# Kernel tuning notes

Hardware: AMD Instinct MI355X
Metric: run time of the kernel (lower is better)

The kernel has to match this reference:

```python
import jax, jax.numpy as jnp
import numpy as np

E = 1024
H = 16
DH = E // H
EPS = 1e-09


def setup_inputs() -> dict:
    key = jax.random.key(0)
    ks = jax.random.split(key, 12)
    B, S = 2, 2048
    scale = 1.0 / np.sqrt(E)
    inp = {
        "query": jax.random.normal(ks[0], (B, S, E), dtype=jnp.float32),
        "key": jax.random.normal(ks[1], (B, S, E), dtype=jnp.float32),
        "value": jax.random.normal(ks[2], (B, S, E), dtype=jnp.float32),
        "mask": jax.random.randint(ks[3], (B, 1, S, S), 0, 2, dtype=jnp.int32),
        "Wq": jax.random.normal(ks[4], (E, E), dtype=jnp.float32) * scale,
        "bq": jnp.zeros((E,), dtype=jnp.float32),
        "Wk": jax.random.normal(ks[5], (E, E), dtype=jnp.float32) * scale,
        "bk": jnp.zeros((E,), dtype=jnp.float32),
        "Wv": jax.random.normal(ks[6], (E, E), dtype=jnp.float32) * scale,
        "bv": jnp.zeros((E,), dtype=jnp.float32),
        "Wo": jax.random.normal(ks[7], (E, E), dtype=jnp.float32) * scale,
        "bo": jnp.zeros((E,), dtype=jnp.float32),
    }
    return inp


def _split_heads(x):
    # [B,S,E] -> [B,H,S,DH]
    B, S, _ = x.shape
    return x.reshape(B, S, H, DH).transpose(0, 2, 1, 3)


def reference(query, key, value, mask, Wq, bq, Wk, bk, Wv, bv, Wo, bo):
    q = _split_heads(query @ Wq.T + bq)
    k = _split_heads(key @ Wk.T + bk)
    v = _split_heads(value @ Wv.T + bv)
    # scores: [B,H,Sq,Sk]; NOTE: original module applies NO softmax.
    scores = jnp.einsum("bhqd,bhkd->bhqk", q, k) / np.sqrt(DH)
    # masked_fill_(mask == 0, epsilon): replace masked positions with 1e-9
    scores = jnp.where(mask == 0, jnp.float32(EPS), scores)
    # dropout p=0.0 (eval) -> identity
    out = jnp.einsum("bhqk,bhkd->bhqd", scores, v)
    B, _, S, _ = out.shape
    out = out.transpose(0, 2, 1, 3).reshape(B, S, E)
    return out @ Wo.T + bo
```

## Files before the change

### kernel.cpp

```cpp
#include <hip/hip_runtime.h>
#include <hip/hip_bf16.h>
#include <stdint.h>
#include <stddef.h>

#define SB 2
#define SS 2048
#define SE 1024
#define SH 16
#define SD 64

typedef __attribute__((ext_vector_type(8))) short bf16x8;
typedef __attribute__((ext_vector_type(4))) float f32x4;

__device__ __forceinline__ short f2bf(float f) {
    union { float f; uint32_t u; } v; v.f = f;
    uint32_t u = v.u;
    uint32_t r = (u + 0x7fffu + ((u >> 16) & 1u)) >> 16;
    return (short)(uint16_t)r;
}

struct CvtArgs {
    const float* src[7];
    short* dst[7];
    int nblk[7];
};

__global__ __launch_bounds__(256) void cvt_bf16(CvtArgs a) {
    const int j = blockIdx.y;
    if (blockIdx.x >= a.nblk[j]) return;
    const size_t i = ((size_t)blockIdx.x * 256 + threadIdx.x) * 8;
    const float* s = a.src[j] + i;
    f32x4 f0 = *(const f32x4*)s;
    f32x4 f1 = *(const f32x4*)(s + 4);
    bf16x8 o;
    o[0] = f2bf(f0[0]); o[1] = f2bf(f0[1]); o[2] = f2bf(f0[2]); o[3] = f2bf(f0[3]);
    o[4] = f2bf(f1[0]); o[5] = f2bf(f1[1]); o[6] = f2bf(f1[2]); o[7] = f2bf(f1[3]);
    *(bf16x8*)(a.dst[j] + i) = o;
}

__global__ __launch_bounds__(256) void pack_mask(const int* __restrict__ m,
                                                 unsigned long long* __restrict__ mp) {
    const int lane = threadIdx.x & 63;
    int wv = (blockIdx.x * 256 + threadIdx.x) >> 6;
    const int NW = SB * SS * (SS / 64);
    const int stride = (gridDim.x * 256) >> 6;
    for (int wd = wv; wd < NW; wd += stride) {
        int v = m[(size_t)wd * 64 + lane];
        unsigned long long b = __ballot(v != 0);
        if (lane == 0) mp[wd] = b;
    }
}

struct GemmJob {
    const short* A; const short* W; const float* bias; void* C;
    int mode;
    float scale;
};

template <bool OUTF32>
__global__ __launch_bounds__(256, 4) void gemm_bf(GemmJob j0, GemmJob j1, GemmJob j2) {
    GemmJob j = (blockIdx.z == 0) ? j0 : (blockIdx.z == 1) ? j1 : j2;
    __shared__ __align__(16) short As[64][72];
    __shared__ __align__(16) short Bs[128][72];

    const int m0 = blockIdx.y * 64;
    const int n0 = blockIdx.x * 128;
    const int tid = threadIdx.x;
    const int lane = tid & 63;
    const int w = tid >> 6;
    const int wm = (w >> 1) * 32;
    const int wn = (w & 1) * 64;
    const int quad = lane >> 4;
    const int l16 = lane & 15;

    f32x4 acc[2][4] = {};
    bf16x8 pa[2], pw[4];

    auto prefetch = [&](int k0) {
#pragma unroll
        for (int r = 0; r < 2; ++r) {
            int c = tid + r * 256; int row = c >> 3; int col = (c & 7) * 8;
            pa[r] = *(const bf16x8*)(j.A + (size_t)(m0 + row) * 1024 + k0 + col);
        }
#pragma unroll
        for (int r = 0; r < 4; ++r) {
            int c = tid + r * 256; int row = c >> 3; int col = (c & 7) * 8;
            pw[r] = *(const bf16x8*)(j.W + (size_t)(n0 + row) * 1024 + k0 + col);
        }
    };

    prefetch(0);
    for (int k0 = 0; k0 < 1024; k0 += 64) {
#pragma unroll
        for (int r = 0; r < 2; ++r) {
            int c = tid + r * 256; int row = c >> 3; int col = (c & 7) * 8;
            *(bf16x8*)&As[row][col] = pa[r];
        }
#pragma unroll
        for (int r = 0; r < 4; ++r) {
            int c = tid + r * 256; int row = c >> 3; int col = (c & 7) * 8;
            *(bf16x8*)&Bs[row][col] = pw[r];
        }
        __syncthreads();
        if (k0 + 64 < 1024) prefetch(k0 + 64);
#pragma unroll
        for (int ks = 0; ks < 2; ++ks) {
            bf16x8 af[2], bfr[4];
#pragma unroll
            for (int mi = 0; mi < 2; ++mi)
                af[mi] = *(const bf16x8*)&As[wm + mi * 16 + l16][ks * 32 + quad * 8];
#pragma unroll
            for (int ni = 0; ni < 4; ++ni)
                bfr[ni] = *(const bf16x8*)&Bs[wn + ni * 16 + l16][ks * 32 + quad * 8];
#pragma unroll
            for (int mi = 0; mi < 2; ++mi)
#pragma unroll
                for (int ni = 0; ni < 4; ++ni)
                    acc[mi][ni] = __builtin_amdgcn_mfma_f32_16x16x32_bf16(
                        af[mi], bfr[ni], acc[mi][ni], 0, 0, 0);
        }
        __syncthreads();
    }

#pragma unroll
    for (int mi = 0; mi < 2; ++mi) {
#pragma unroll
        for (int ni = 0; ni < 4; ++ni) {
            int n = n0 + wn + ni * 16 + l16;
            float bv = j.bias[n];
#pragma unroll
            for (int r = 0; r < 4; ++r) {
                int m = m0 + wm + mi * 16 + quad * 4 + r;
                float v = (acc[mi][ni][r] + bv) * j.scale;
                if (OUTF32) {
                    ((float*)j.C)[(size_t)m * 1024 + n] = v;
                } else {
                    short o = f2bf(v);
                    short* C = (short*)j.C;
                    if (j.mode == 0) {
                        C[(size_t)m * 1024 + n] = o;
                    } else {
                        int b = m >> 11, s = m & 2047;
                        int hh = n >> 6, d = n & 63;
                        if (j.mode == 1)
                            C[(((size_t)(b * SH + hh) * SS) + s) * SD + d] = o;
                        else
                            C[(((size_t)(b * SH + hh) * SD) + d) * SS + s] = o;
                    }
                }
            }
        }
    }
}

__global__ __launch_bounds__(256, 2) void attn_nosoftmax(
    const short* __restrict__ Q,
    const short* __restrict__ Kk,
    const short* __restrict__ Vt,
    const unsigned long long* __restrict__ Mp,
    short* __restrict__ O) {
    __shared__ __align__(16) short Ks[128][72];
    __shared__ __align__(16) short Ssm[128 * 136];

    const int bh = blockIdx.y;
    const int qt = blockIdx.x;
    const int b = bh >> 4;
    const int h = bh & 15;
    const int q0 = qt * 128;

    const short* qbase = Q + (size_t)bh * SS * SD;
    const short* kbase = Kk + (size_t)bh * SS * SD;
    const short* vbase = Vt + (size_t)bh * SD * SS;
    const unsigned long long* mbase = Mp + (size_t)b * SS * (SS / 64);

    const int tid = threadIdx.x;
    const int lane = tid & 63;
    const int w = tid >> 6;
    const int quad = lane >> 4;
    const int l16 = lane & 15;
    const int wm = (w >> 1) * 64;
    const int wn = (w & 1) * 64;

    bf16x8 qa[4][2];
#pragma unroll
    for (int mi = 0; mi < 4; ++mi)
#pragma unroll
        for (int ks = 0; ks < 2; ++ks)
            qa[mi][ks] = *(const bf16x8*)(qbase +
                (size_t)(q0 + wm + mi * 16 + l16) * SD + ks * 32 + quad * 8);

    f32x4 oacc[2][4] = {};
    const int pq = w * 32;

    bf16x8 kpf[4];
    auto kload = [&](int kk0) {
#pragma unroll
        for (int r = 0; r < 4; ++r) {
            int c = tid + r * 256; int row = c >> 3; int col = (c & 7) * 8;
            kpf[r] = *(const bf16x8*)(kbase + (size_t)(kk0 + row) * SD + col);
        }
    };
    auto kstore = [&]() {
#pragma unroll
        for (int r = 0; r < 4; ++r) {
            int c = tid + r * 256; int row = c >> 3; int col = (c & 7) * 8;
            *(bf16x8*)&Ks[row][col] = kpf[r];
        }
    };

    kload(0);
    kstore();
    __syncthreads();

    for (int k0 = 0; k0 < SS; k0 += 128) {
        int kpf0 = (k0 + 128 < SS) ? k0 + 128 : k0;
        kload(kpf0);

        f32x4 sacc[4][4] = {};
#pragma unroll
        for (int ks = 0; ks < 2; ++ks) {
            bf16x8 kb[4];
#pragma unroll
            for (int ni = 0; ni < 4; ++ni)
                kb[ni] = *(const bf16x8*)&Ks[wn + ni * 16 + l16][ks * 32 + quad * 8];
#pragma unroll
            for (int mi = 0; mi < 4; ++mi)
#pragma unroll
                for (int ni = 0; ni < 4; ++ni)
                    sacc[mi][ni] = __builtin_amdgcn_mfma_f32_16x16x32_bf16(
                        qa[mi][ks], kb[ni], sacc[mi][ni], 0, 0, 0);
        }

        const int mcol = ((k0 + wn) >> 6);
#pragma unroll
        for (int mi = 0; mi < 4; ++mi) {
            int qrow_l = wm + mi * 16 + quad * 4;
#pragma unroll
            for (int r = 0; r < 4; ++r) {
                unsigned long long mwd =
                    mbase[(size_t)(q0 + qrow_l + r) * (SS / 64) + mcol];
                unsigned long long sh = mwd >> l16;
                short* dst = &Ssm[(qrow_l + r) * 136 + wn + l16];
#pragma unroll
                for (int ni = 0; ni < 4; ++ni) {
                    uint32_t bit = (uint32_t)(sh >> (16 * ni)) & 1u;
                    float v = bit ? sacc[mi][ni][r] : 0.0f;
                    dst[ni * 16] = f2bf(v);
                }
            }
        }
        __syncthreads();

        kstore();

#pragma unroll
        for (int ks2 = 0; ks2 < 4; ++ks2) {
            bf16x8 sa[2], vb[4];
#pragma unroll
            for (int mi2 = 0; mi2 < 2; ++mi2)
                sa[mi2] = *(const bf16x8*)&Ssm[(pq + mi2 * 16 + l16) * 136 +
                                               ks2 * 32 + quad * 8];
#pragma unroll
            for (int ni = 0; ni < 4; ++ni)
                vb[ni] = *(const bf16x8*)(vbase + (size_t)(ni * 16 + l16) * SS +
                                          k0 + ks2 * 32 + quad * 8);
#pragma unroll
            for (int mi2 = 0; mi2 < 2; ++mi2)
#pragma unroll
                for (int ni = 0; ni < 4; ++ni)
                    oacc[mi2][ni] = __builtin_amdgcn_mfma_f32_16x16x32_bf16(
                        sa[mi2], vb[ni], oacc[mi2][ni], 0, 0, 0);
        }
        __syncthreads();
    }

#pragma unroll
    for (int mi2 = 0; mi2 < 2; ++mi2) {
#pragma unroll
        for (int ni = 0; ni < 4; ++ni) {
            int d = ni * 16 + l16;
#pragma unroll
            for (int r = 0; r < 4; ++r) {
                int qg = q0 + pq + mi2 * 16 + quad * 4 + r;
                O[((size_t)b * SS + qg) * SE + h * SD + d] =
                    f2bf(oacc[mi2][ni][r]);
            }
        }
    }
}

extern "C" void kernel_launch(void* const* d_in, const int* in_sizes, int n_in,
                              void* d_out, int out_size, void* d_ws,
                              size_t ws_size, hipStream_t stream) {
    const float* query = (const float*)d_in[0];
    const float* key   = (const float*)d_in[1];
    const float* value = (const float*)d_in[2];
    const int*   mask  = (const int*)d_in[3];
    float* out = (float*)d_out;

    const size_t NEL = (size_t)SB * SS * SE;
    unsigned long long* Mp = (unsigned long long*)d_out;
    short* mb   = (short*)d_in[3];
    short* qbf  = mb;
    short* kbf  = mb + NEL;
    short* vbf  = mb + 2 * NEL;
    short* Wqb  = mb + 3 * NEL;
    short* Wkb  = Wqb + SE * SE;
    short* Wvb  = Wkb + SE * SE;
    short* Wob  = Wvb + SE * SE;
    short* Qb   = (short*)d_in[0];
    short* Om   = (short*)d_in[0] + NEL;
    short* Kb   = (short*)d_in[1];
    short* Vtb  = (short*)d_in[2];

    dim3 tblk(256);

    pack_mask<<<dim3(1024), tblk, 0, stream>>>(mask, Mp);

    CvtArgs ca;
    ca.src[0] = query; ca.dst[0] = qbf; ca.nblk[0] = 2048;
    ca.src[1] = key;   ca.dst[1] = kbf; ca.nblk[1] = 2048;
    ca.src[2] = value; ca.dst[2] = vbf; ca.nblk[2] = 2048;
    ca.src[3] = (const float*)d_in[4];  ca.dst[3] = Wqb; ca.nblk[3] = 512;
    ca.src[4] = (const float*)d_in[6];  ca.dst[4] = Wkb; ca.nblk[4] = 512;
    ca.src[5] = (const float*)d_in[8];  ca.dst[5] = Wvb; ca.nblk[5] = 512;
    ca.src[6] = (const float*)d_in[10]; ca.dst[6] = Wob; ca.nblk[6] = 512;
    cvt_bf16<<<dim3(2048, 7), tblk, 0, stream>>>(ca);

    GemmJob jq{qbf, Wqb, (const float*)d_in[5], Qb,  1, 0.125f};
    GemmJob jv{vbf, Wvb, (const float*)d_in[9], Vtb, 2, 1.0f};
    GemmJob jk{kbf, Wkb, (const float*)d_in[7], Kb,  1, 1.0f};
    gemm_bf<false><<<dim3(8, 64, 3), tblk, 0, stream>>>(jq, jv, jk);

    attn_nosoftmax<<<dim3(SS / 128, SB * SH), tblk, 0, stream>>>(Qb, Kb, Vtb, Mp, Om);

    GemmJob jo{Om, Wob, (const float*)d_in[11], out, 0, 1.0f};
    gemm_bf<true><<<dim3(8, 64, 1), tblk, 0, stream>>>(jo, jo, jo);
}
```

Before: 325.0 us.

## Rewrite attention to register-resident scores and use direct-to-LDS GEMM loads

The attention kernel is restructured to 64-query tiles, one 16-row slab per wave. It computes S^T = K·Q^T so the masked scores can go straight from MFMA accumulators into the A operand of the PV MFMA, with no LDS round trip. K and V tiles are double-buffered in LDS, and the mask is packed transposed so each lane reads one contiguous 64-bit word. The projection GEMMs move to 128x128 tiles that load via global_load_lds. They drop the register prefetch and use an unpadded LDS layout, which risks bank conflicts and leaves load latency exposed between the two barriers.

Result: faster. 288.8 us (-11.1%).

```diff
diff --git a/kernel.cpp b/kernel.cpp
--- a/kernel.cpp
+++ b/kernel.cpp
@@ -17,6 +17,20 @@
     uint32_t u = v.u;
     uint32_t r = (u + 0x7fffu + ((u >> 16) & 1u)) >> 16;
     return (short)(uint16_t)r;
+}
+
+__device__ __forceinline__ uint32_t pkmask(float a, float b, uint32_t bits) {
+    union { float f; uint32_t u; } ua, ub;
+    ua.f = a; ub.f = b;
+    uint32_t ra = (bits & 1u) ? (ua.u + 0x7fffu + ((ua.u >> 16) & 1u)) : 0u;
+    uint32_t rb = (bits & 2u) ? (ub.u + 0x7fffu + ((ub.u >> 16) & 1u)) : 0u;
+    return (rb & 0xffff0000u) | (ra >> 16);
+}
+
+__device__ __forceinline__ void gld16(const short* g, short* l) {
+    __builtin_amdgcn_global_load_lds(
+        (const __attribute__((address_space(1))) unsigned int*)g,
+        (__attribute__((address_space(3))) unsigned int*)l, 16, 0, 0);
 }
 
 struct CvtArgs {
@@ -46,8 +60,13 @@
     const int stride = (gridDim.x * 256) >> 6;
     for (int wd = wv; wd < NW; wd += stride) {
         int v = m[(size_t)wd * 64 + lane];
-        unsigned long long b = __ballot(v != 0);
-        if (lane == 0) mp[wd] = b;
+        unsigned long long bb = __ballot(v != 0);
+        if (lane == 0) {
+            int b = wd >> 16;
+            int q = (wd >> 5) & 2047;
+            int kw = wd & 31;
+            mp[((size_t)b << 16) + kw * 2048 + q] = bb;
+        }
     }
 }
 
@@ -58,62 +77,44 @@
 };
 
 template <bool OUTF32>
-__global__ __launch_bounds__(256, 4) void gemm_bf(GemmJob j0, GemmJob j1, GemmJob j2) {
+__global__ __launch_bounds__(256, 3) void gemm128(GemmJob j0, GemmJob j1, GemmJob j2) {
     GemmJob j = (blockIdx.z == 0) ? j0 : (blockIdx.z == 1) ? j1 : j2;
-    __shared__ __align__(16) short As[64][72];
-    __shared__ __align__(16) short Bs[128][72];
-
-    const int m0 = blockIdx.y * 64;
+    __shared__ short As[128 * 64];
+    __shared__ short Bs[128 * 64];
+
+    const int m0 = blockIdx.y * 128;
     const int n0 = blockIdx.x * 128;
     const int tid = threadIdx.x;
     const int lane = tid & 63;
     const int w = tid >> 6;
-    const int wm = (w >> 1) * 32;
+    const int wm = (w >> 1) * 64;
     const int wn = (w & 1) * 64;
     const int quad = lane >> 4;
     const int l16 = lane & 15;
 
-    f32x4 acc[2][4] = {};
-    bf16x8 pa[2], pw[4];
-
-    auto prefetch = [&](int k0) {
-#pragma unroll
-        for (int r = 0; r < 2; ++r) {
-            int c = tid + r * 256; int row = c >> 3; int col = (c & 7) * 8;
-            pa[r] = *(const bf16x8*)(j.A + (size_t)(m0 + row) * 1024 + k0 + col);
-        }
-#pragma unroll
-        for (int r = 0; r < 4; ++r) {
-            int c = tid + r * 256; int row = c >> 3; int col = (c & 7) * 8;
-            pw[r] = *(const bf16x8*)(j.W + (size_t)(n0 + row) * 1024 + k0 + col);
-        }
-    };
-
-    prefetch(0);
+    f32x4 acc[4][4] = {};
+
     for (int k0 = 0; k0 < 1024; k0 += 64) {
 #pragma unroll
-        for (int r = 0; r < 2; ++r) {
-            int c = tid + r * 256; int row = c >> 3; int col = (c & 7) * 8;
-            *(bf16x8*)&As[row][col] = pa[r];
-        }
-#pragma unroll
-        for (int r = 0; r < 4; ++r) {
-            int c = tid + r * 256; int row = c >> 3; int col = (c & 7) * 8;
-            *(bf16x8*)&Bs[row][col] = pw[r];
+        for (int i = 0; i < 4; ++i) {
+            int ch = lane + 64 * (w * 4 + i);
+            int row = ch >> 3;
+            int col = (ch & 7) * 8;
+            gld16(j.A + (size_t)(m0 + row) * 1024 + k0 + col, &As[(w * 4 + i) * 512]);
+            gld16(j.W + (size_t)(n0 + row) * 1024 + k0 + col, &Bs[(w * 4 + i) * 512]);
         }
         __syncthreads();
-        if (k0 + 64 < 1024) prefetch(k0 + 64);
 #pragma unroll
         for (int ks = 0; ks < 2; ++ks) {
-            bf16x8 af[2], bfr[4];
-#pragma unroll
-            for (int mi = 0; mi < 2; ++mi)
-                af[mi] = *(const bf16x8*)&As[wm + mi * 16 + l16][ks * 32 + quad * 8];
+            bf16x8 af[4], bfr[4];
+#pragma unroll
+            for (int mi = 0; mi < 4; ++mi)
+                af[mi] = *(const bf16x8*)&As[(wm + mi * 16 + l16) * 64 + ks * 32 + quad * 8];
 #pragma unroll
             for (int ni = 0; ni < 4; ++ni)
-                bfr[ni] = *(const bf16x8*)&Bs[wn + ni * 16 + l16][ks * 32 + quad * 8];
-#pragma unroll
-            for (int mi = 0; mi < 2; ++mi)
+                bfr[ni] = *(const bf16x8*)&Bs[(wn + ni * 16 + l16) * 64 + ks * 32 + quad * 8];
+#pragma unroll
+            for (int mi = 0; mi < 4; ++mi)
 #pragma unroll
                 for (int ni = 0; ni < 4; ++ni)
                     acc[mi][ni] = __builtin_amdgcn_mfma_f32_16x16x32_bf16(
@@ -123,7 +124,7 @@
     }
 
 #pragma unroll
-    for (int mi = 0; mi < 2; ++mi) {
+    for (int mi = 0; mi < 4; ++mi) {
 #pragma unroll
         for (int ni = 0; ni < 4; ++ni) {
             int n = n0 + wn + ni * 16 + l16;
@@ -153,138 +154,116 @@
     }
 }
 
-__global__ __launch_bounds__(256, 2) void attn_nosoftmax(
+__global__ __launch_bounds__(256, 4) void attn2(
     const short* __restrict__ Q,
     const short* __restrict__ Kk,
     const short* __restrict__ Vt,
-    const unsigned long long* __restrict__ Mp,
+    const unsigned long long* __restrict__ MpT,
     short* __restrict__ O) {
-    __shared__ __align__(16) short Ks[128][72];
-    __shared__ __align__(16) short Ssm[128 * 136];
-
+    __shared__ __align__(16) short Ks[2][64 * 72];
+    __shared__ __align__(16) short Vs[2][64 * 72];
+
+    const int qt = blockIdx.x;
     const int bh = blockIdx.y;
-    const int qt = blockIdx.x;
     const int b = bh >> 4;
     const int h = bh & 15;
-    const int q0 = qt * 128;
+    const int q0 = qt * 64;
 
     const short* qbase = Q + (size_t)bh * SS * SD;
     const short* kbase = Kk + (size_t)bh * SS * SD;
     const short* vbase = Vt + (size_t)bh * SD * SS;
-    const unsigned long long* mbase = Mp + (size_t)b * SS * (SS / 64);
+    const unsigned long long* mTb = MpT + ((size_t)b << 16);
 
     const int tid = threadIdx.x;
     const int lane = tid & 63;
     const int w = tid >> 6;
     const int quad = lane >> 4;
     const int l16 = lane & 15;
-    const int wm = (w >> 1) * 64;
-    const int wn = (w & 1) * 64;
-
-    bf16x8 qa[4][2];
-#pragma unroll
-    for (int mi = 0; mi < 4; ++mi)
-#pragma unroll
-        for (int ks = 0; ks < 2; ++ks)
-            qa[mi][ks] = *(const bf16x8*)(qbase +
-                (size_t)(q0 + wm + mi * 16 + l16) * SD + ks * 32 + quad * 8);
-
-    f32x4 oacc[2][4] = {};
-    const int pq = w * 32;
-
-    bf16x8 kpf[4];
-    auto kload = [&](int kk0) {
+    const int qw = q0 + w * 16;
+
+    const bf16x8 qf0 = *(const bf16x8*)(qbase + (size_t)(qw + l16) * SD + quad * 8);
+    const bf16x8 qf1 = *(const bf16x8*)(qbase + (size_t)(qw + l16) * SD + 32 + quad * 8);
+
+    f32x4 oacc[4] = {};
+
+    bf16x8 kpf[2], vpf[2];
+    int prow[2], pcol[2];
+#pragma unroll
+    for (int r = 0; r < 2; ++r) {
+        int ch = tid + r * 256;
+        prow[r] = ch >> 3;
+        pcol[r] = (ch & 7) * 8;
+    }
+    auto loadKV = [&](int k0) {
+#pragma unroll
+        for (int r = 0; r < 2; ++r) {
+            kpf[r] = *(const bf16x8*)(kbase + (size_t)(k0 + prow[r]) * SD + pcol[r]);
+            vpf[r] = *(const bf16x8*)(vbase + (size_t)prow[r] * SS + k0 + pcol[r]);
+        }
+    };
+    auto storeKV = [&](int buf) {
+#pragma unroll
+        for (int r = 0; r < 2; ++r) {
+            *(bf16x8*)&Ks[buf][prow[r] * 72 + pcol[r]] = kpf[r];
+            *(bf16x8*)&Vs[buf][prow[r] * 72 + pcol[r]] = vpf[r];
+        }
+    };
+
+    loadKV(0);
+    int cur = 0;
+
+    for (int k0 = 0; k0 < SS; k0 += 64) {
+        storeKV(cur);
+        if (k0 + 64 < SS) loadKV(k0 + 64);
+        unsigned long long w64 = mTb[(k0 >> 6) * 2048 + qw + l16];
+        __syncthreads();
+
+        const short* KsB = &Ks[cur][0];
+        const short* VsB = &Vs[cur][0];
+#pragma unroll
+        for (int p = 0; p < 2; ++p) {
+            const int s0 = p * 2, s1 = p * 2 + 1;
+            bf16x8 a00 = *(const bf16x8*)&KsB[(s0 * 16 + l16) * 72 + quad * 8];
+            bf16x8 a01 = *(const bf16x8*)&KsB[(s0 * 16 + l16) * 72 + 32 + quad * 8];
+            bf16x8 a10 = *(const bf16x8*)&KsB[(s1 * 16 + l16) * 72 + quad * 8];
+            bf16x8 a11 = *(const bf16x8*)&KsB[(s1 * 16 + l16) * 72 + 32 + quad * 8];
+            f32x4 sA = {}, sB = {};
+            sA = __builtin_amdgcn_mfma_f32_16x16x32_bf16(a00, qf0, sA, 0, 0, 0);
+            sA = __builtin_amdgcn_mfma_f32_16x16x32_bf16(a01, qf1, sA, 0, 0, 0);
+            sB = __builtin_amdgcn_mfma_f32_16x16x32_bf16(a10, qf0, sB, 0, 0, 0);
+            sB = __builtin_amdgcn_mfma_f32_16x16x32_bf16(a11, qf1, sB, 0, 0, 0);
+
+            uint32_t sh0 = (uint32_t)(w64 >> (s0 * 16 + quad * 4));
+            uint32_t sh1 = (uint32_t)(w64 >> (s1 * 16 + quad * 4));
+            union { uint32_t d[4]; bf16x8 v; } scf;
+            scf.d[0] = pkmask(sA[0], sA[1], sh0);
+            scf.d[1] = pkmask(sA[2], sA[3], sh0 >> 2);
+            scf.d[2] = pkmask(sB[0], sB[1], sh1);
+            scf.d[3] = pkmask(sB[2], sB[3], sh1 >> 2);
+
+#pragma unroll
+            for (int di = 0; di < 4; ++di) {
+                union { uint32_t d[4]; bf16x8 v; } vb;
+                const uint32_t* vlo =
+                    (const uint32_t*)&VsB[(di * 16 + l16) * 72 + s0 * 16 + quad * 4];
+                const uint32_t* vhi =
+                    (const uint32_t*)&VsB[(di * 16 + l16) * 72 + s1 * 16 + quad * 4];
+                vb.d[0] = vlo[0]; vb.d[1] = vlo[1];
+                vb.d[2] = vhi[0]; vb.d[3] = vhi[1];
+                oacc[di] = __builtin_amdgcn_mfma_f32_16x16x32_bf16(
+                    scf.v, vb.v, oacc[di], 0, 0, 0);
+            }
+        }
+        cur ^= 1;
+    }
+
+#pragma unroll
+    for (int di = 0; di < 4; ++di) {
+        int d = di * 16 + l16;
 #pragma unroll
         for (int r = 0; r < 4; ++r) {
-            int c = tid + r * 256; int row = c >> 3; int col = (c & 7) * 8;
-            kpf[r] = *(const bf16x8*)(kbase + (size_t)(kk0 + row) * SD + col);
-        }
-    };
-    auto kstore = [&]() {
-#pragma unroll
-        for (int r = 0; r < 4; ++r) {
-            int c = tid + r * 256; int row = c >> 3; int col = (c & 7) * 8;
-            *(bf16x8*)&Ks[row][col] = kpf[r];
-        }
-    };
-
-    kload(0);
-    kstore();
-    __syncthreads();
-
-    for (int k0 = 0; k0 < SS; k0 += 128) {
-        int kpf0 = (k0 + 128 < SS) ? k0 + 128 : k0;
-        kload(kpf0);
-
-        f32x4 sacc[4][4] = {};
-#pragma unroll
-        for (int ks = 0; ks < 2; ++ks) {
-            bf16x8 kb[4];
-#pragma unroll
-            for (int ni = 0; ni < 4; ++ni)
-                kb[ni] = *(const bf16x8*)&Ks[wn + ni * 16 + l16][ks * 32 + quad * 8];
-#pragma unroll
-            for (int mi = 0; mi < 4; ++mi)
-#pragma unroll
-                for (int ni = 0; ni < 4; ++ni)
-                    sacc[mi][ni] = __builtin_amdgcn_mfma_f32_16x16x32_bf16(
-                        qa[mi][ks], kb[ni], sacc[mi][ni], 0, 0, 0);
-        }
-
-        const int mcol = ((k0 + wn) >> 6);
-#pragma unroll
-        for (int mi = 0; mi < 4; ++mi) {
-            int qrow_l = wm + mi * 16 + quad * 4;
-#pragma unroll
-            for (int r = 0; r < 4; ++r) {
-                unsigned long long mwd =
-                    mbase[(size_t)(q0 + qrow_l + r) * (SS / 64) + mcol];
-                unsigned long long sh = mwd >> l16;
-                short* dst = &Ssm[(qrow_l + r) * 136 + wn + l16];
-#pragma unroll
-                for (int ni = 0; ni < 4; ++ni) {
-                    uint32_t bit = (uint32_t)(sh >> (16 * ni)) & 1u;
-                    float v = bit ? sacc[mi][ni][r] : 0.0f;
-                    dst[ni * 16] = f2bf(v);
-                }
-            }
-        }
-        __syncthreads();
-
-        kstore();
-
-#pragma unroll
-        for (int ks2 = 0; ks2 < 4; ++ks2) {
-            bf16x8 sa[2], vb[4];
-#pragma unroll
-            for (int mi2 = 0; mi2 < 2; ++mi2)
-                sa[mi2] = *(const bf16x8*)&Ssm[(pq + mi2 * 16 + l16) * 136 +
-                                               ks2 * 32 + quad * 8];
-#pragma unroll
-            for (int ni = 0; ni < 4; ++ni)
-                vb[ni] = *(const bf16x8*)(vbase + (size_t)(ni * 16 + l16) * SS +
-                                          k0 + ks2 * 32 + quad * 8);
-#pragma unroll
-            for (int mi2 = 0; mi2 < 2; ++mi2)
-#pragma unroll
-                for (int ni = 0; ni < 4; ++ni)
-                    oacc[mi2][ni] = __builtin_amdgcn_mfma_f32_16x16x32_bf16(
-                        sa[mi2], vb[ni], oacc[mi2][ni], 0, 0, 0);
-        }
-        __syncthreads();
-    }
-
-#pragma unroll
-    for (int mi2 = 0; mi2 < 2; ++mi2) {
-#pragma unroll
-        for (int ni = 0; ni < 4; ++ni) {
-            int d = ni * 16 + l16;
-#pragma unroll
-            for (int r = 0; r < 4; ++r) {
-                int qg = q0 + pq + mi2 * 16 + quad * 4 + r;
-                O[((size_t)b * SS + qg) * SE + h * SD + d] =
-                    f2bf(oacc[mi2][ni][r]);
-            }
+            int qg = qw + quad * 4 + r;
+            O[((size_t)b * SS + qg) * SE + h * SD + d] = f2bf(oacc[di][r]);
         }
     }
 }
@@ -330,10 +309,10 @@
     GemmJob jq{qbf, Wqb, (const float*)d_in[5], Qb,  1, 0.125f};
     GemmJob jv{vbf, Wvb, (const float*)d_in[9], Vtb, 2, 1.0f};
     GemmJob jk{kbf, Wkb, (const float*)d_in[7], Kb,  1, 1.0f};
-    gemm_bf<false><<<dim3(8, 64, 3), tblk, 0, stream>>>(jq, jv, jk);
-
-    attn_nosoftmax<<<dim3(SS / 128, SB * SH), tblk, 0, stream>>>(Qb, Kb, Vtb, Mp, Om);
+    gemm128<false><<<dim3(8, 32, 3), tblk, 0, stream>>>(jq, jv, jk);
+
+    attn2<<<dim3(SS / 64, SB * SH), tblk, 0, stream>>>(Qb, Kb, Vtb, Mp, Om);
 
     GemmJob jo{Om, Wob, (const float*)d_in[11], out, 0, 1.0f};
-    gemm_bf<true><<<dim3(8, 64, 1), tblk, 0, stream>>>(jo, jo, jo);
-}
+    gemm128<true><<<dim3(8, 32, 1), tblk, 0, stream>>>(jo, jo, jo);
+}
```
